# Kernel optimization log

Hardware: AMD Instinct MI355X
Metric: run time of the kernel (lower is better)

## Reference

```python
import jax, jax.numpy as jnp
import numpy as np

B, D_IN, D_H, D_BOT, D_EXP, N_CLS = 8192, 1024, 2048, 512, 1024, 10


def _w(key, shape):
    return jax.random.normal(key, shape, dtype=jnp.float32) * 0.02


def setup_inputs() -> dict:
    key = jax.random.key(0)
    ks = jax.random.split(key, 16)
    return {
        "x": jax.random.normal(ks[0], (B, D_IN), dtype=jnp.float32),
        "labels": jax.random.randint(ks[1], (B,), 0, N_CLS, dtype=jnp.int32),
        # encoder: 1024 -> 2048 -> 512 (ReLU after each)
        "W1": _w(ks[2], (D_IN, D_H)), "b1": jnp.zeros((D_H,), jnp.float32),
        "W2": _w(ks[3], (D_H, D_BOT)), "b2": jnp.zeros((D_BOT,), jnp.float32),
        # per-class expert MLPs (identical shapes, stacked): 512 -> 1024 -> 512, ReLU after each
        "EW1": _w(ks[4], (N_CLS, D_BOT, D_EXP)), "Eb1": jnp.zeros((N_CLS, D_EXP), jnp.float32),
        "EW2": _w(ks[5], (N_CLS, D_EXP, D_BOT)), "Eb2": jnp.zeros((N_CLS, D_BOT), jnp.float32),
        # decoder: 512 -> 2048 (ReLU) -> 1024 (no final activation)
        "DW1": _w(ks[6], (D_BOT, D_H)), "Db1": jnp.zeros((D_H,), jnp.float32),
        "DW2": _w(ks[7], (D_H, D_IN)), "Db2": jnp.zeros((D_IN,), jnp.float32),
    }


def reference(x, labels, W1, b1, W2, b2, EW1, Eb1, EW2, Eb2, DW1, Db1, DW2, Db2):
    # encoder
    h = jax.nn.relu(x @ W1 + b1)           # [B, 2048]
    h = jax.nn.relu(h @ W2 + b2)           # [B, 512]
    # class-routed experts: compute all experts densely, then gather by label
    he = jax.nn.relu(jnp.einsum('bi,eio->beo', h, EW1) + Eb1[None])   # [B, E, 1024]
    he = jax.nn.relu(jnp.einsum('beh,eho->beo', he, EW2) + Eb2[None]) # [B, E, 512]
    sel = jnp.take_along_axis(he, labels[:, None, None].astype(jnp.int32), axis=1)[:, 0]  # [B, 512]
    # decoder (activation after first layer only)
    d = jax.nn.relu(sel @ DW1 + Db1)       # [B, 2048]
    out = d @ DW2 + Db2                    # [B, 1024]
    return out
```

## Files before the change

### kernel.cpp

```cpp
#include <hip/hip_runtime.h>
#include <hip/hip_bf16.h>
#include <stdint.h>

typedef __attribute__((ext_vector_type(8))) short bf16x8;
typedef __attribute__((ext_vector_type(4))) float f32x4;

__device__ __forceinline__ unsigned short f2bf(float f) {
  unsigned int u = __float_as_uint(f);
  u += 0x7fff + ((u >> 16) & 1);
  return (unsigned short)(u >> 16);
}

__device__ __forceinline__ void gload16(const void* g, void* l) {
  __builtin_amdgcn_global_load_lds(
      (const __attribute__((address_space(1))) void*)g,
      (__attribute__((address_space(3))) void*)l, 16, 0, 0);
}

#define Bsz   8192
#define D_IN  1024
#define D_H   2048
#define D_BOT 512
#define D_EXP 1024
#define N_CLS 10

__global__ __launch_bounds__(1024) void k_route(const int* __restrict__ lab,
                                                int* __restrict__ counts,
                                                int* __restrict__ starts,
                                                int* __restrict__ perm) {
  __shared__ int scnt[N_CLS], scur[N_CLS];
  const int t = threadIdx.x;
  if (t < N_CLS) scnt[t] = 0;
  __syncthreads();
  int myl[8];
#pragma unroll
  for (int i = 0; i < 8; ++i) {
    myl[i] = lab[t * 8 + i];
    atomicAdd(&scnt[myl[i]], 1);
  }
  __syncthreads();
  if (t == 0) {
    int s = 0;
    for (int e = 0; e < N_CLS; ++e) {
      starts[e] = s; scur[e] = s; counts[e] = scnt[e]; s += scnt[e];
    }
  }
  __syncthreads();
#pragma unroll
  for (int i = 0; i < 8; ++i) {
    int p = atomicAdd(&scur[myl[i]], 1);
    perm[p] = t * 8 + i;
  }
}

__global__ void k_cvt(const float* __restrict__ in, unsigned short* __restrict__ out) {
  int i = (blockIdx.x * blockDim.x + threadIdx.x) * 8;
  const float4* p = (const float4*)(in + i);
  float4 a = p[0], b = p[1];
  uint4 o;
  o.x = (unsigned)f2bf(a.x) | ((unsigned)f2bf(a.y) << 16);
  o.y = (unsigned)f2bf(a.z) | ((unsigned)f2bf(a.w) << 16);
  o.z = (unsigned)f2bf(b.x) | ((unsigned)f2bf(b.y) << 16);
  o.w = (unsigned)f2bf(b.z) | ((unsigned)f2bf(b.w) << 16);
  *(uint4*)(out + i) = o;
}

__global__ void k_transpose_cvt(const float* __restrict__ in, unsigned short* __restrict__ out,
                                int K, int N) {
  __shared__ float tile[32][33];
  size_t eoff = (size_t)blockIdx.z * K * N;
  in  += eoff;
  out += eoff;
  int n0 = blockIdx.x * 32, k0 = blockIdx.y * 32;
  int tx = threadIdx.x, ty = threadIdx.y;
#pragma unroll
  for (int i = 0; i < 4; i++) {
    int k = ty + i * 8;
    tile[k][tx] = in[(size_t)(k0 + k) * N + n0 + tx];
  }
  __syncthreads();
#pragma unroll
  for (int i = 0; i < 4; i++) {
    int n = ty + i * 8;
    out[(size_t)(n0 + n) * K + k0 + tx] = f2bf(tile[tx][n]);
  }
}


template <int TBM, int TBN, int WM, int WN,
          bool RELU, bool BF16OUT, bool GROUPED, bool SCATTER, bool GATHER>
__global__ __launch_bounds__(256) void k_gemm(
    const unsigned short* __restrict__ A,
    const unsigned short* __restrict__ WT,
    const float* __restrict__ bias,
    void* __restrict__ Cv,
    int M, int N, int K,
    const int* __restrict__ starts, const int* __restrict__ counts,
    const int* __restrict__ perm) {
  constexpr int FM = TBM / WM / 16;
  constexpr int FN = TBN / WN / 16;
  constexpr int ALOADS = TBM / 64;
  constexpr int BLOADS = TBN / 64;
  constexpr int LDS_LD = ALOADS + BLOADS;

  const int nby = gridDim.y;
  const int nwg = gridDim.x * nby;
  int orig = blockIdx.x + gridDim.x * blockIdx.y;
  int q = nwg >> 3, r = nwg & 7;
  int xcd = orig & 7, idx = orig >> 3;
  int wg = (xcd < r ? xcd * (q + 1) : r * (q + 1) + (xcd - r) * q) + idx;
  int bx = wg / nby, by = wg % nby;

  int Meff, start = 0, mo;
  const unsigned short* Wp = WT;
  const float* biasp = bias;
  if (GROUPED) {
    int bxr = bx;
    int found = 0;
#pragma unroll
    for (int e = 0; e < N_CLS; ++e) {
      int c = counts[e];
      int nb = (c + TBM - 1) / TBM;
      if (!found && bxr < nb) {
        found = 1; Meff = c; start = starts[e]; mo = bxr * TBM;
        Wp = WT + (size_t)e * N * K; biasp = bias + (size_t)e * N;
      }
      if (!found) bxr -= nb;
    }
    if (!found) return;
    if (!GATHER) A += (size_t)start * K;
  } else {
    Meff = M; mo = bx * TBM;
  }
  const int n0 = by * TBN;

  __shared__ __align__(16) unsigned short As[3][TBM * 32];
  __shared__ __align__(16) unsigned short Bs[3][TBN * 32];

  const int t = threadIdx.x;
  const int l = t & 63;
  const int w = t >> 6;
  const int wm = (w / WN) * (TBM / WM);
  const int wn = (w % WN) * (TBN / WN);

  const int srow = t >> 2;
  const int scol = (t & 3) * 8;
  const unsigned short* ag[ALOADS];
  const unsigned short* bg[BLOADS];
#pragma unroll
  for (int i = 0; i < ALOADS; ++i) {
    int arow = mo + srow + i * 64;
    if (GROUPED) arow = arow < Meff ? arow : Meff - 1;
    int srcrow = GATHER ? perm[start + arow] : arow;
    ag[i] = A + (size_t)srcrow * K + scol;
  }
#pragma unroll
  for (int i = 0; i < BLOADS; ++i)
    bg[i] = Wp + (size_t)(n0 + srow + i * 64) * K + scol;

  auto STAGE = [&](int buf) {
#pragma unroll
    for (int i = 0; i < ALOADS; ++i) {
      gload16(ag[i], &As[buf][t * 8 + i * 2048]);
      ag[i] += 32;
    }
#pragma unroll
    for (int i = 0; i < BLOADS; ++i) {
      gload16(bg[i], &Bs[buf][t * 8 + i * 2048]);
      bg[i] += 32;
    }
  };

  f32x4 acc[FM][FN] = {};

  const int nt = K / 32;
  STAGE(0);
  STAGE(1);
  for (int tI = 0; tI < nt; ++tI) {
    if (tI + 1 < nt)
      asm volatile("s_waitcnt vmcnt(%0)" :: "i"(LDS_LD) : "memory");
    else
      asm volatile("s_waitcnt vmcnt(0)" ::: "memory");
    __builtin_amdgcn_s_barrier();
    __builtin_amdgcn_sched_barrier(0);
    if (tI + 2 < nt) STAGE((tI + 2) % 3);

    const int cur = tI % 3;
    bf16x8 af[FM], bfr[FN];
#pragma unroll
    for (int i = 0; i < FM; ++i)
      af[i] = *(const bf16x8*)(&As[cur][(wm + i * 16 + (l & 15)) * 32 + (l >> 4) * 8]);
#pragma unroll
    for (int i = 0; i < FN; ++i)
      bfr[i] = *(const bf16x8*)(&Bs[cur][(wn + i * 16 + (l & 15)) * 32 + (l >> 4) * 8]);
#pragma unroll
    for (int mi = 0; mi < FM; ++mi)
#pragma unroll
      for (int ni = 0; ni < FN; ++ni)
        acc[mi][ni] = __builtin_amdgcn_mfma_f32_16x16x32_bf16(af[mi], bfr[ni], acc[mi][ni], 0, 0, 0);
  }

  const int cb = n0 + wn + (l & 15);
#pragma unroll
  for (int ni = 0; ni < FN; ++ni) {
    int c = cb + ni * 16;
    float bv = biasp[c];
#pragma unroll
    for (int mi = 0; mi < FM; ++mi) {
#pragma unroll
      for (int j = 0; j < 4; ++j) {
        int rl = wm + mi * 16 + ((l >> 4) << 2) + j;
        int re = mo + rl;
        if (GROUPED && re >= Meff) continue;
        float v = acc[mi][ni][j] + bv;
        if (RELU) v = fmaxf(v, 0.0f);
        int orow;
        if (SCATTER)      orow = perm[start + re];
        else if (GROUPED) orow = start + re;
        else              orow = re;
        if (BF16OUT) ((unsigned short*)Cv)[(size_t)orow * N + c] = f2bf(v);
        else         ((float*)Cv)[(size_t)orow * N + c] = v;
      }
    }
  }
}

#define GX_GROUPED 74

extern "C" void kernel_launch(void* const* d_in, const int* in_sizes, int n_in,
                              void* d_out, int out_size, void* d_ws, size_t ws_size,
                              hipStream_t stream) {
  const float* x      = (const float*)d_in[0];
  const int*   labels = (const int*)d_in[1];
  const float* W1  = (const float*)d_in[2];  const float* b1  = (const float*)d_in[3];
  const float* W2  = (const float*)d_in[4];  const float* b2  = (const float*)d_in[5];
  const float* EW1 = (const float*)d_in[6];  const float* Eb1 = (const float*)d_in[7];
  const float* EW2 = (const float*)d_in[8];  const float* Eb2 = (const float*)d_in[9];
  const float* DW1 = (const float*)d_in[10]; const float* Db1 = (const float*)d_in[11];
  const float* DW2 = (const float*)d_in[12]; const float* Db2 = (const float*)d_in[13];
  float* out = (float*)d_out;

  char* ws = (char*)d_ws;
  size_t o = 0;
  unsigned short* W1T  = (unsigned short*)(ws + o); o += (size_t)D_IN * D_H * 2;
  unsigned short* W2T  = (unsigned short*)(ws + o); o += (size_t)D_H * D_BOT * 2;
  unsigned short* EW1T = (unsigned short*)(ws + o); o += (size_t)N_CLS * D_BOT * D_EXP * 2;
  unsigned short* EW2T = (unsigned short*)(ws + o); o += (size_t)N_CLS * D_EXP * D_BOT * 2;
  unsigned short* DW1T = (unsigned short*)(ws + o); o += (size_t)D_BOT * D_H * 2;
  unsigned short* DW2T = (unsigned short*)(ws + o); o += (size_t)D_H * D_IN * 2;
  unsigned short* xb   = (unsigned short*)(ws + o); o += (size_t)Bsz * D_IN * 2;
  unsigned short* e1p  = xb;
  unsigned short* actA = (unsigned short*)(ws + o); o += (size_t)Bsz * D_H * 2;
  unsigned short* h2   = (unsigned short*)(ws + o); o += (size_t)Bsz * D_BOT * 2;
  unsigned short* sel  = (unsigned short*)(ws + o); o += (size_t)Bsz * D_BOT * 2;
  int* counts = (int*)(ws + o);
  int* starts = counts + 16;
  int* perm   = counts + 64;

  k_route<<<1, 1024, 0, stream>>>(labels, counts, starts, perm);

  k_cvt<<<(Bsz * D_IN) / (256 * 8), 256, 0, stream>>>(x, xb);
  k_transpose_cvt<<<dim3(D_H / 32, D_IN / 32, 1),  dim3(32, 8), 0, stream>>>(W1, W1T, D_IN, D_H);
  k_transpose_cvt<<<dim3(D_BOT / 32, D_H / 32, 1), dim3(32, 8), 0, stream>>>(W2, W2T, D_H, D_BOT);
  k_transpose_cvt<<<dim3(D_EXP / 32, D_BOT / 32, N_CLS), dim3(32, 8), 0, stream>>>(EW1, EW1T, D_BOT, D_EXP);
  k_transpose_cvt<<<dim3(D_BOT / 32, D_EXP / 32, N_CLS), dim3(32, 8), 0, stream>>>(EW2, EW2T, D_EXP, D_BOT);
  k_transpose_cvt<<<dim3(D_H / 32, D_BOT / 32, 1), dim3(32, 8), 0, stream>>>(DW1, DW1T, D_BOT, D_H);
  k_transpose_cvt<<<dim3(D_IN / 32, D_H / 32, 1),  dim3(32, 8), 0, stream>>>(DW2, DW2T, D_H, D_IN);

  k_gemm<128, 128, 2, 2, true, true, false, false, false><<<dim3(Bsz / 128, D_H / 128), 256, 0, stream>>>(
      xb, W1T, b1, actA, Bsz, D_H, D_IN, nullptr, nullptr, nullptr);
  k_gemm<128, 64, 4, 1, true, true, false, false, false><<<dim3(Bsz / 128, D_BOT / 64), 256, 0, stream>>>(
      actA, W2T, b2, h2, Bsz, D_BOT, D_H, nullptr, nullptr, nullptr);

  k_gemm<128, 128, 2, 2, true, true, true, false, true><<<dim3(GX_GROUPED, D_EXP / 128), 256, 0, stream>>>(
      h2, EW1T, Eb1, e1p, Bsz, D_EXP, D_BOT, starts, counts, perm);
  k_gemm<128, 64, 4, 1, true, true, true, true, false><<<dim3(GX_GROUPED, D_BOT / 64), 256, 0, stream>>>(
      e1p, EW2T, Eb2, sel, Bsz, D_BOT, D_EXP, starts, counts, perm);

  k_gemm<128, 128, 2, 2, true, true, false, false, false><<<dim3(Bsz / 128, D_H / 128), 256, 0, stream>>>(
      sel, DW1T, Db1, actA, Bsz, D_H, D_BOT, nullptr, nullptr, nullptr);
  k_gemm<128, 128, 2, 2, false, false, false, false, false><<<dim3(Bsz / 128, D_IN / 128), 256, 0, stream>>>(
      actA, DW2T, Db2, out, Bsz, D_IN, D_H, nullptr, nullptr, nullptr);
}
```

Measured before the change: 265.5 us.

## Add 8-wave 256x256 GEMM kernel with swizzled LDS for dense layers

Adds a new 512-thread GEMM kernel with large 256x256 (or 128x256) tiles, BK=64, XOR-swizzled LDS layout, XCD-aware block remapping, and a quadrant-ordered MFMA schedule using setprio and barriers. It replaces the encoder first layer and both decoder layers with this kernel. The aim is more operand reuse per LDS load, fewer bank conflicts, and better L2 locality across XCDs. In exchange it uses more LDS and registers per block and launches fewer blocks, which can lower occupancy or leave the wave count on the GPU poorly balanced.

```diff
diff --git a/kernel.cpp b/kernel.cpp
--- a/kernel.cpp
+++ b/kernel.cpp
@@ -86,6 +86,182 @@
   }
 }
 
+template <int BM, int BN, bool RELU, bool BF16OUT>
+__global__ __launch_bounds__(512, 2) void k_gemm8(
+    const unsigned short* __restrict__ A,
+    const unsigned short* __restrict__ WT,
+    const float* __restrict__ bias,
+    void* __restrict__ Cv,
+    int M, int N, int K) {
+  constexpr int WROWS = BM / 2;
+  constexpr int QR = WROWS / 2;
+  constexpr int FMq = QR / 16;
+  constexpr int ACH = BM / 64;
+  constexpr int BCH = BN / 64;
+
+  const int nby = gridDim.y;
+  const int nwg = gridDim.x * nby;
+  int orig = blockIdx.x + gridDim.x * blockIdx.y;
+  int q = nwg >> 3, r = nwg & 7;
+  int xcd = orig & 7, idx = orig >> 3;
+  int wg = (xcd < r ? xcd * (q + 1) : r * (q + 1) + (xcd - r) * q) + idx;
+  int bx = wg / nby, by = wg % nby;
+  const int m0 = bx * BM, n0 = by * BN;
+
+  __shared__ __align__(16) unsigned short As[2][BM * 64];
+  __shared__ __align__(16) unsigned short Bs[2][BN * 64];
+
+  const int t = threadIdx.x;
+  const int l = t & 63;
+  const int w = t >> 6;
+  const int wm = w >> 2, wn = w & 3;
+
+  const int rl = t >> 3;
+  const int sl16 = (t & 7) ^ (rl & 7);
+  const unsigned short* asrc[ACH];
+  const unsigned short* bsrc[BCH];
+#pragma unroll
+  for (int i = 0; i < ACH; ++i)
+    asrc[i] = A + (size_t)(m0 + i * 64 + rl) * K + sl16 * 8;
+#pragma unroll
+  for (int i = 0; i < BCH; ++i)
+    bsrc[i] = WT + (size_t)(n0 + i * 64 + rl) * K + sl16 * 8;
+  const int dst = t * 8;
+
+  auto STAGE = [&](int kt, int buf) {
+#pragma unroll
+    for (int i = 0; i < ACH; ++i)
+      gload16(asrc[i] + kt * 64, &As[buf][i * 4096 + dst]);
+#pragma unroll
+    for (int i = 0; i < BCH; ++i)
+      gload16(bsrc[i] + kt * 64, &Bs[buf][i * 4096 + dst]);
+  };
+
+  f32x4 acc[2][2][FMq][2] = {};
+  bf16x8 af[FMq][2];
+  bf16x8 bq[2][2][2];
+
+  const int la = l & 15;
+  const int ko = l >> 4;
+  const int arow0 = wm * WROWS + la;
+  const int brow0 = wn * 64 + la;
+
+  const int nt = K / 64;
+  STAGE(0, 0);
+
+  for (int kt = 0; kt < nt; ++kt) {
+    const int cur = kt & 1;
+    const char* Ab = (const char*)As[cur];
+    const char* Bb = (const char*)Bs[cur];
+
+    asm volatile("s_waitcnt vmcnt(0)" ::: "memory");
+    __builtin_amdgcn_s_barrier();
+    if (kt + 1 < nt) STAGE(kt + 1, cur ^ 1);
+    __builtin_amdgcn_sched_barrier(0);
+
+#pragma unroll
+    for (int fm = 0; fm < FMq; ++fm)
+#pragma unroll
+      for (int ks = 0; ks < 2; ++ks) {
+        int row = arow0 + fm * 16;
+        int s = ks * 4 + ko;
+        af[fm][ks] = *(const bf16x8*)(Ab + (row << 7) + ((s ^ (row & 7)) << 4));
+      }
+#pragma unroll
+    for (int fn = 0; fn < 2; ++fn)
+#pragma unroll
+      for (int ks = 0; ks < 2; ++ks) {
+        int row = brow0 + fn * 16;
+        int s = ks * 4 + ko;
+        bq[0][fn][ks] = *(const bf16x8*)(Bb + (row << 7) + ((s ^ (row & 7)) << 4));
+      }
+    __builtin_amdgcn_s_setprio(1);
+#pragma unroll
+    for (int fm = 0; fm < FMq; ++fm)
+#pragma unroll
+      for (int fn = 0; fn < 2; ++fn)
+#pragma unroll
+        for (int ks = 0; ks < 2; ++ks)
+          acc[0][0][fm][fn] = __builtin_amdgcn_mfma_f32_16x16x32_bf16(
+              af[fm][ks], bq[0][fn][ks], acc[0][0][fm][fn], 0, 0, 0);
+    __builtin_amdgcn_s_setprio(0);
+    __builtin_amdgcn_s_barrier();
+
+#pragma unroll
+    for (int fn = 0; fn < 2; ++fn)
+#pragma unroll
+      for (int ks = 0; ks < 2; ++ks) {
+        int row = brow0 + 32 + fn * 16;
+        int s = ks * 4 + ko;
+        bq[1][fn][ks] = *(const bf16x8*)(Bb + (row << 7) + ((s ^ (row & 7)) << 4));
+      }
+    __builtin_amdgcn_s_setprio(1);
+#pragma unroll
+    for (int fm = 0; fm < FMq; ++fm)
+#pragma unroll
+      for (int fn = 0; fn < 2; ++fn)
+#pragma unroll
+        for (int ks = 0; ks < 2; ++ks)
+          acc[0][1][fm][fn] = __builtin_amdgcn_mfma_f32_16x16x32_bf16(
+              af[fm][ks], bq[1][fn][ks], acc[0][1][fm][fn], 0, 0, 0);
+    __builtin_amdgcn_s_setprio(0);
+    __builtin_amdgcn_s_barrier();
+
+#pragma unroll
+    for (int fm = 0; fm < FMq; ++fm)
+#pragma unroll
+      for (int ks = 0; ks < 2; ++ks) {
+        int row = arow0 + QR + fm * 16;
+        int s = ks * 4 + ko;
+        af[fm][ks] = *(const bf16x8*)(Ab + (row << 7) + ((s ^ (row & 7)) << 4));
+      }
+    __builtin_amdgcn_s_setprio(1);
+#pragma unroll
+    for (int fm = 0; fm < FMq; ++fm)
+#pragma unroll
+      for (int fn = 0; fn < 2; ++fn)
+#pragma unroll
+        for (int ks = 0; ks < 2; ++ks)
+          acc[1][0][fm][fn] = __builtin_amdgcn_mfma_f32_16x16x32_bf16(
+              af[fm][ks], bq[0][fn][ks], acc[1][0][fm][fn], 0, 0, 0);
+    __builtin_amdgcn_s_setprio(0);
+    __builtin_amdgcn_s_barrier();
+
+    __builtin_amdgcn_s_setprio(1);
+#pragma unroll
+    for (int fm = 0; fm < FMq; ++fm)
+#pragma unroll
+      for (int fn = 0; fn < 2; ++fn)
+#pragma unroll
+        for (int ks = 0; ks < 2; ++ks)
+          acc[1][1][fm][fn] = __builtin_amdgcn_mfma_f32_16x16x32_bf16(
+              af[fm][ks], bq[1][fn][ks], acc[1][1][fm][fn], 0, 0, 0);
+    __builtin_amdgcn_s_setprio(0);
+  }
+  asm volatile("s_waitcnt vmcnt(0)" ::: "memory");
+
+  const int crow0 = m0 + wm * WROWS;
+  const int ccol0 = n0 + wn * 64;
+#pragma unroll
+  for (int qn = 0; qn < 2; ++qn)
+#pragma unroll
+    for (int fn = 0; fn < 2; ++fn) {
+      int c = ccol0 + qn * 32 + fn * 16 + la;
+      float bv = bias[c];
+#pragma unroll
+      for (int qm = 0; qm < 2; ++qm)
+#pragma unroll
+        for (int fm = 0; fm < FMq; ++fm)
+#pragma unroll
+          for (int j = 0; j < 4; ++j) {
+            int rr = crow0 + qm * QR + fm * 16 + (ko << 2) + j;
+            float v = acc[qm][qn][fm][fn][j] + bv;
+            if (RELU) v = fmaxf(v, 0.0f);
+            if (BF16OUT) ((unsigned short*)Cv)[(size_t)rr * N + c] = f2bf(v);
+            else         ((float*)Cv)[(size_t)rr * N + c] = v;
+          }
+    }
+}
 
 template <int TBM, int TBN, int WM, int WN,
           bool RELU, bool BF16OUT, bool GROUPED, bool SCATTER, bool GATHER>
@@ -209,8 +385,8 @@
     for (int mi = 0; mi < FM; ++mi) {
 #pragma unroll
       for (int j = 0; j < 4; ++j) {
-        int rl = wm + mi * 16 + ((l >> 4) << 2) + j;
-        int re = mo + rl;
+        int rl2 = wm + mi * 16 + ((l >> 4) << 2) + j;
+        int re = mo + rl2;
         if (GROUPED && re >= Meff) continue;
         float v = acc[mi][ni][j] + bv;
         if (RELU) v = fmaxf(v, 0.0f);
@@ -267,8 +443,8 @@
   k_transpose_cvt<<<dim3(D_H / 32, D_BOT / 32, 1), dim3(32, 8), 0, stream>>>(DW1, DW1T, D_BOT, D_H);
   k_transpose_cvt<<<dim3(D_IN / 32, D_H / 32, 1),  dim3(32, 8), 0, stream>>>(DW2, DW2T, D_H, D_IN);
 
-  k_gemm<128, 128, 2, 2, true, true, false, false, false><<<dim3(Bsz / 128, D_H / 128), 256, 0, stream>>>(
-      xb, W1T, b1, actA, Bsz, D_H, D_IN, nullptr, nullptr, nullptr);
+  k_gemm8<256, 256, true, true><<<dim3(Bsz / 256, D_H / 256), 512, 0, stream>>>(
+      xb, W1T, b1, actA, Bsz, D_H, D_IN);
   k_gemm<128, 64, 4, 1, true, true, false, false, false><<<dim3(Bsz / 128, D_BOT / 64), 256, 0, stream>>>(
       actA, W2T, b2, h2, Bsz, D_BOT, D_H, nullptr, nullptr, nullptr);
 
@@ -277,8 +453,8 @@
   k_gemm<128, 64, 4, 1, true, true, true, true, false><<<dim3(GX_GROUPED, D_BOT / 64), 256, 0, stream>>>(
       e1p, EW2T, Eb2, sel, Bsz, D_BOT, D_EXP, starts, counts, perm);
 
-  k_gemm<128, 128, 2, 2, true, true, false, false, false><<<dim3(Bsz / 128, D_H / 128), 256, 0, stream>>>(
-      sel, DW1T, Db1, actA, Bsz, D_H, D_BOT, nullptr, nullptr, nullptr);
-  k_gemm<128, 128, 2, 2, false, false, false, false, false><<<dim3(Bsz / 128, D_IN / 128), 256, 0, stream>>>(
-      actA, DW2T, Db2, out, Bsz, D_IN, D_H, nullptr, nullptr, nullptr);
-}
+  k_gemm8<256, 256, true, true><<<dim3(Bsz / 256, D_H / 256), 512, 0, stream>>>(
+      sel, DW1T, Db1, actA, Bsz, D_H, D_BOT);
+  k_gemm8<128, 256, false, false><<<dim3(Bsz / 128, D_IN / 256), 512, 0, stream>>>(
+      actA, DW2T, Db2, out, Bsz, D_IN, D_H);
+}
```

After: 252.5 us. -4.9%, faster.
